# Kernel tuning notes

Hardware: AMD Instinct MI355X
Metric: run time of the kernel (lower is better)

The kernel has to match this reference:

```python
import jax, jax.numpy as jnp
import numpy as np

D = 1024        # embed_dim
H = 16          # num_heads
HD = D // H     # head_dim
R = 8           # LoRA rank
LORA_SCALE = 16.0 / R  # alpha / r
W_BITS = 8
A_BITS = 8


def fake_quant(x, bits):
    # symmetric per-tensor fake quantization with straight-through estimator
    qmax = 2.0 ** (bits - 1) - 1.0
    scale = jnp.maximum(jnp.max(jnp.abs(x)) / qmax, 1e-8)
    q = jnp.round(x / scale) * scale
    return x + jax.lax.stop_gradient(q - x)


def quant_lora_linear(x, W, b, A, B):
    # QuantizeLinear: fake-quant activations (a_bits) and weights (w_bits)
    base = jnp.matmul(fake_quant(x, A_BITS), fake_quant(W, W_BITS).T) + b
    # active LoRA adapter: x @ A^T @ B^T * scaling (dropout=0)
    lora = jnp.matmul(jnp.matmul(x, A.T), B.T) * LORA_SCALE
    return base + lora


def setup_inputs() -> dict:
    key = jax.random.key(0)
    ks = jax.random.split(key, 20)
    bsz, seq = 2, 2048
    inp = {
        "hidden_states": jax.random.normal(ks[0], (bsz, seq, D), jnp.float32),
        "attention_mask": jnp.ones((bsz, seq), jnp.float32),
    }
    i = 1
    for name in ("q", "k", "v", "out"):
        inp[f"{name}_W"] = jax.random.normal(ks[i], (D, D), jnp.float32) * 0.02; i += 1
        inp[f"{name}_b"] = jnp.zeros((D,), jnp.float32)
        inp[f"{name}_A"] = jax.random.normal(ks[i], (R, D), jnp.float32) * 0.01; i += 1
        inp[f"{name}_B"] = jax.random.normal(ks[i], (D, R), jnp.float32) * 0.01; i += 1
    return inp


def reference(hidden_states, attention_mask,
              q_W, q_b, q_A, q_B,
              k_W, k_b, k_A, k_B,
              v_W, v_b, v_A, v_B,
              out_W, out_b, out_A, out_B):
    bsz, seq, _ = hidden_states.shape

    q = quant_lora_linear(hidden_states, q_W, q_b, q_A, q_B)
    k = quant_lora_linear(hidden_states, k_W, k_b, k_A, k_B)
    v = quant_lora_linear(hidden_states, v_W, v_b, v_A, v_B)

    # (b, s, D) -> (b, H, s, HD)
    def shape_heads(x):
        return x.reshape(bsz, seq, H, HD).transpose(0, 2, 1, 3)

    q, k, v = shape_heads(q), shape_heads(k), shape_heads(v)

    scores = jnp.einsum("bhqd,bhkd->bhqk", q, k) / jnp.sqrt(jnp.float32(HD))
    # additive mask: (1 - mask) * -10000, broadcast over (b, 1, 1, s)
    scores = scores + (1.0 - attention_mask)[:, None, None, :] * -10000.0
    probs = jax.nn.softmax(scores, axis=-1)

    attn = jnp.einsum("bhqk,bhkd->bhqd", probs, v)
    attn = attn.transpose(0, 2, 1, 3).reshape(bsz, seq, D)
    return quant_lora_linear(attn, out_W, out_b, out_A, out_B)
```

## Files before the change

kernel.cpp:

```cpp
#include <hip/hip_runtime.h>
#include <stdint.h>

typedef __attribute__((ext_vector_type(8))) short short8;
typedef __attribute__((ext_vector_type(4))) float f32x4;
typedef __attribute__((ext_vector_type(4))) int int32x4;
typedef unsigned short ushort_t;
typedef signed char i8_t;

#define SEQ   2048
#define BSZ   2
#define DIM   1024
#define NHEAD 16
#define HDIM  64
#define MROWS (BSZ*SEQ)

__device__ __forceinline__ ushort_t f2bf(float f) {
  unsigned u = __float_as_uint(f);
  unsigned r = u + 0x7fffu + ((u >> 16) & 1u);
  return (ushort_t)(r >> 16);
}

__device__ __forceinline__ unsigned cvt_pk_bf16(float lo, float hi) {
  unsigned r;
  asm("v_cvt_pk_bf16_f32 %0, %1, %2" : "=v"(r) : "v"(lo), "v"(hi));
  return r;
}

__device__ __forceinline__ float fast_exp2(float x) {
#if __has_builtin(__builtin_amdgcn_exp2f)
  return __builtin_amdgcn_exp2f(x);
#else
  return exp2f(x);
#endif
}

__device__ __forceinline__ int pack4i8(float a, float b, float c, float d) {
  int ia = (int)rintf(a), ib = (int)rintf(b), ic = (int)rintf(c), id = (int)rintf(d);
  return (ia & 255) | ((ib & 255) << 8) | ((ic & 255) << 16) | (id << 24);
}

typedef __attribute__((address_space(1))) void gas_void;
typedef __attribute__((address_space(3))) void las_void;
__device__ __forceinline__ void gll16(const void* g, void* l, int lane) {
#if __has_builtin(__builtin_amdgcn_global_load_lds)
  __builtin_amdgcn_global_load_lds((gas_void*)g, (las_void*)l, 16, 0, 0);
#else
  ((int4*)l)[lane] = *(const int4*)g;
#endif
}

__device__ __forceinline__ void amax_reduce_store(float m, unsigned* slot) {
  __shared__ float wred[4];
  int wv = threadIdx.x >> 6, lane = threadIdx.x & 63;
#pragma unroll
  for (int off = 32; off > 0; off >>= 1) m = fmaxf(m, __shfl_down(m, off));
  if (lane == 0) wred[wv] = m;
  __syncthreads();
  if (threadIdx.x == 0) {
    float r = fmaxf(fmaxf(wred[0], wred[1]), fmaxf(wred[2], wred[3]));
    atomicMax(slot, __float_as_uint(r));
  }
}

__global__ __launch_bounds__(256) void amax5_kernel(
    const float* __restrict__ x, const float* w0, const float* w1,
    const float* w2, const float* w3, int n4x, int n4w,
    unsigned* __restrict__ slots) {
  int y = blockIdx.y;
  const float* p = (y == 0) ? x : (y == 1) ? w0 : (y == 2) ? w1 : (y == 3) ? w2 : w3;
  int n4 = (y == 0) ? n4x : n4w;
  const float4* x4 = (const float4*)p;
  float m = 0.f;
  for (int i = blockIdx.x * blockDim.x + threadIdx.x; i < n4; i += gridDim.x * blockDim.x) {
    float4 v = x4[i];
    m = fmaxf(m, fmaxf(fmaxf(fabsf(v.x), fabsf(v.y)), fmaxf(fabsf(v.z), fabsf(v.w))));
  }
  amax_reduce_store(m, slots + y);
}

__global__ __launch_bounds__(256) void quant4_kernel(const float* w0, const float* w1,
                                                     const float* w2, const float* w3,
                                                     i8_t* q0, i8_t* q1,
                                                     i8_t* q2, i8_t* q3,
                                                     int n4, const unsigned* __restrict__ slots) {
  int y = blockIdx.y;
  const float* x = (y == 0) ? w0 : (y == 1) ? w1 : (y == 2) ? w2 : w3;
  i8_t* qc = (y == 0) ? q0 : (y == 1) ? q1 : (y == 2) ? q2 : q3;
  float amax = __uint_as_float(slots[y + 1]);
  float s = fmaxf(amax / 127.0f, 1e-8f);
  float inv = 1.0f / s;
  const float4* x4 = (const float4*)x;
  int* q4 = (int*)qc;
  for (int i = blockIdx.x * blockDim.x + threadIdx.x; i < n4; i += gridDim.x * blockDim.x) {
    float4 v = x4[i];
    q4[i] = pack4i8(v.x * inv, v.y * inv, v.z * inv, v.w * inv);
  }
}

template <int NL>
__global__ __launch_bounds__(256) void lora_quant_kernel(
    const float* __restrict__ x, const unsigned* __restrict__ slot,
    i8_t* __restrict__ xc,
    const float* __restrict__ A0, const float* __restrict__ A1, const float* __restrict__ A2,
    float* __restrict__ t0, float* __restrict__ t1, float* __restrict__ t2) {
  const int row = blockIdx.x;
  const int tid = threadIdx.x;
  const int k0 = tid * 4;
  float amax = __uint_as_float(*slot);
  float s = fmaxf(amax / 127.0f, 1e-8f);
  float inv = 1.0f / s;

  float4 xv = *(const float4*)&x[(size_t)row * DIM + k0];
  *(int*)&xc[(size_t)row * DIM + k0] = pack4i8(xv.x * inv, xv.y * inv, xv.z * inv, xv.w * inv);

  float p[NL * 8];
#pragma unroll
  for (int r = 0; r < 8; r++) {
    float4 a = *(const float4*)&A0[r * DIM + k0];
    p[r] = xv.x * a.x + xv.y * a.y + xv.z * a.z + xv.w * a.w;
    if (NL > 1) {
      float4 a1 = *(const float4*)&A1[r * DIM + k0];
      p[8 + r] = xv.x * a1.x + xv.y * a1.y + xv.z * a1.z + xv.w * a1.w;
    }
    if (NL > 2) {
      float4 a2 = *(const float4*)&A2[r * DIM + k0];
      p[16 + r] = xv.x * a2.x + xv.y * a2.y + xv.z * a2.z + xv.w * a2.w;
    }
  }
#pragma unroll
  for (int j = 0; j < NL * 8; j++) {
    float v = p[j];
#pragma unroll
    for (int off = 32; off > 0; off >>= 1) v += __shfl_down(v, off);
    p[j] = v;
  }
  __shared__ float red[4][24];
  int wv = tid >> 6, lane = tid & 63;
  if (lane == 0) {
#pragma unroll
    for (int j = 0; j < NL * 8; j++) red[wv][j] = p[j];
  }
  __syncthreads();
  if (tid < NL * 8) {
    int j = tid;
    float sv = red[0][j] + red[1][j] + red[2][j] + red[3][j];
    float* tp = (j < 8) ? t0 : ((j < 16) ? t1 : t2);
    tp[(size_t)row * 8 + (j & 7)] = sv;
  }
}

template <bool BF16OUT, int BN>
__device__ __forceinline__ void proj_body(
    const i8_t* __restrict__ Ac, const i8_t* __restrict__ Wc,
    const unsigned* __restrict__ sxslot, const unsigned* __restrict__ swslot,
    const float* __restrict__ bias, const float* __restrict__ t,
    const float* __restrict__ Bl, void* __restrict__ Cout,
    int m0, int n0) {
  __shared__ alignas(16) i8_t Asb[128 * 128];
  __shared__ alignas(16) i8_t Bsb[BN * 128];
  __shared__ float Ts[128 * 8];
  __shared__ float Bls[BN * 8];
  __shared__ float biass[BN];

  const int tid = threadIdx.x;
  constexpr int NJ = BN / 32;
  constexpr int BITS = BN / 32;

  for (int i = tid; i < 128 * 8; i += 256) Ts[i] = t[(size_t)m0 * 8 + i];
  for (int i = tid; i < BN * 8; i += 256) Bls[i] = Bl[(size_t)n0 * 8 + i];
  if (tid < BN) biass[tid] = bias[n0 + tid];

  int32x4 acc[4][NJ];
#pragma unroll
  for (int i = 0; i < 4; i++)
#pragma unroll
    for (int j = 0; j < NJ; j++) {
      acc[i][j][0] = 0; acc[i][j][1] = 0; acc[i][j][2] = 0; acc[i][j][3] = 0;
    }

  const int wv = tid >> 6, lane = tid & 63;
  const int wr = wv >> 1, wc = wv & 1;
  const int l15 = lane & 15, hi = lane >> 4;
  const int lr8 = lane >> 3, lc8 = lane & 7;

  for (int kt = 0; kt < 8; kt++) {
    const int k0 = kt * 128;
#pragma unroll
    for (int j = 0; j < 4; j++) {
      int row = wv * 32 + j * 8 + lr8;
      int cs = lc8 ^ (row & 7);
      gll16(&Ac[(size_t)(m0 + row) * DIM + k0 + cs * 16], &Asb[(wv * 32 + j * 8) * 128], lane);
    }
#pragma unroll
    for (int j = 0; j < BITS; j++) {
      int row = wv * (BN / 4) + j * 8 + lr8;
      int cs = lc8 ^ (row & 7);
      gll16(&Wc[(size_t)(n0 + row) * DIM + k0 + cs * 16], &Bsb[(wv * (BN / 4) + j * 8) * 128], lane);
    }
    __syncthreads();
#pragma unroll
    for (int ks = 0; ks < 2; ks++) {
      int32x4 a[4], b[NJ];
#pragma unroll
      for (int i = 0; i < 4; i++) {
        int row = wr * 64 + i * 16 + l15;
        a[i] = *(const int32x4*)&Asb[row * 128 + (((ks * 4 + hi) ^ (row & 7))) * 16];
      }
#pragma unroll
      for (int j = 0; j < NJ; j++) {
        int col = wc * (BN / 2) + j * 16 + l15;
        b[j] = *(const int32x4*)&Bsb[col * 128 + (((ks * 4 + hi) ^ (col & 7))) * 16];
      }
      __builtin_amdgcn_s_setprio(1);
#pragma unroll
      for (int i = 0; i < 4; i++)
#pragma unroll
        for (int j = 0; j < NJ; j++)
          acc[i][j] = __builtin_amdgcn_mfma_i32_16x16x64_i8(a[i], b[j], acc[i][j], 0, 0, 0);
      __builtin_amdgcn_s_setprio(0);
    }
    __syncthreads();
  }

  float sx = fmaxf(__uint_as_float(*sxslot) / 127.0f, 1e-8f);
  float sw = fmaxf(__uint_as_float(*swslot) / 127.0f, 1e-8f);
  float ss = sx * sw;
#pragma unroll
  for (int i = 0; i < 4; i++) {
#pragma unroll
    for (int rr = 0; rr < 4; rr++) {
      int rl = wr * 64 + i * 16 + hi * 4 + rr;
      float tv[8];
#pragma unroll
      for (int q = 0; q < 8; q++) tv[q] = Ts[rl * 8 + q];
#pragma unroll
      for (int j = 0; j < NJ; j++) {
        int cl = wc * (BN / 2) + j * 16 + l15;
        float lr = 0.f;
#pragma unroll
        for (int q = 0; q < 8; q++) lr += tv[q] * Bls[cl * 8 + q];
        float val = (float)acc[i][j][rr] * ss + biass[cl] + 2.0f * lr;
        if (BF16OUT)
          ((ushort_t*)Cout)[(size_t)(m0 + rl) * DIM + n0 + cl] = f2bf(val);
        else
          ((float*)Cout)[(size_t)(m0 + rl) * DIM + n0 + cl] = val;
      }
    }
  }
}

struct ProjSet {
  const i8_t* W; const unsigned* sw; const float* bias;
  const float* t; const float* Bl; ushort_t* out;
};

__global__ __launch_bounds__(256) void proj_qkv_kernel(
    const i8_t* __restrict__ Ac, const unsigned* __restrict__ sxslot,
    ProjSet pq, ProjSet pk, ProjSet pv) {
  ProjSet P = (blockIdx.z == 0) ? pq : (blockIdx.z == 1) ? pk : pv;
  proj_body<true, 128>(Ac, P.W, sxslot, P.sw, P.bias, P.t, P.Bl, P.out,
                       blockIdx.y * 128, blockIdx.x * 128);
}

__global__ __launch_bounds__(256) void proj_out_kernel(
    const i8_t* __restrict__ Ac, const i8_t* __restrict__ Wc,
    const unsigned* __restrict__ sxslot, const unsigned* __restrict__ swslot,
    const float* __restrict__ bias, const float* __restrict__ t,
    const float* __restrict__ Bl, float* __restrict__ Cout) {
  proj_body<false, 64>(Ac, Wc, sxslot, swslot, bias, t, Bl, Cout,
                       blockIdx.y * 128, blockIdx.x * 64);
}

__global__ __launch_bounds__(256) void vtrans_kernel(const ushort_t* __restrict__ vb,
                                                     ushort_t* __restrict__ vT) {
  __shared__ alignas(16) ushort_t Lt[64 * 72];
  const int s0 = blockIdx.x * 64;
  const int bh = blockIdx.y;
  const int b = bh >> 4, h = bh & 15;
  const int tid = threadIdx.x;
#pragma unroll
  for (int it = 0; it < 2; it++) {
    int g = it * 256 + tid;
    int r = g >> 3, c = g & 7;
    *(int4*)&Lt[r * 72 + c * 8] =
        *(const int4*)&vb[(size_t)(b * SEQ + s0 + r) * DIM + h * 64 + c * 8];
  }
  __syncthreads();
#pragma unroll
  for (int it = 0; it < 2; it++) {
    int g = it * 256 + tid;
    int d = g >> 3, c = g & 7;
    union { int4 v; ushort_t u[8]; } out;
#pragma unroll
    for (int j = 0; j < 8; j++) out.u[j] = Lt[(c * 8 + j) * 72 + d];
    *(int4*)&vT[((size_t)bh * 64 + d) * SEQ + s0 + c * 8] = out.v;
  }
}

__global__ __launch_bounds__(256) void attn9_kernel(
    const ushort_t* __restrict__ qb, const ushort_t* __restrict__ kb,
    const ushort_t* __restrict__ vT, const float* __restrict__ mask,
    float* __restrict__ obuf, unsigned* __restrict__ amax_slot) {
  __shared__ alignas(16) ushort_t Ks[2][64 * 64];
  __shared__ alignas(16) ushort_t Vs[2][64 * 64];
  __shared__ alignas(16) ushort_t Ps[128 * 72];
  __shared__ alignas(16) float maskv[2][64];
  __shared__ float wmax[4];

  const float LOG2E = 1.44269504088896f;
  const float SCL2 = 0.125f * LOG2E;
  const float THR2 = 8.0f * LOG2E;

  const int lin = blockIdx.x;
  const int logical = (lin & 7) * 64 + (lin >> 3);
  const int bh = logical >> 4;
  const int qt = logical & 15;
  const int b = bh >> 4, h = bh & 15;
  const size_t tokbase = (size_t)b * SEQ;
  const int q0 = qt * 128;

  const int tid = threadIdx.x;
  const int wv = tid >> 6, lane = tid & 63, l15 = lane & 15, hi = lane >> 4;
  const int sr = tid >> 3, sc = tid & 7;
  const int sslot = (sc ^ (sr & 7)) * 8;
  const int sslot2 = (sc ^ ((sr + 32) & 7)) * 8;

  short8 qf[2][2];
#pragma unroll
  for (int rb = 0; rb < 2; rb++)
#pragma unroll
    for (int ks = 0; ks < 2; ks++) {
      int row = q0 + wv * 32 + rb * 16 + l15;
      qf[rb][ks] = *(const short8*)&qb[(tokbase + row) * DIM + h * 64 + ks * 32 + hi * 8];
    }

  float mo[2], ls[2];
  f32x4 o[2][4];
#pragma unroll
  for (int rb = 0; rb < 2; rb++) { mo[rb] = -1e30f; ls[rb] = 0.f; }
#pragma unroll
  for (int rb = 0; rb < 2; rb++)
#pragma unroll
    for (int d = 0; d < 4; d++) { o[rb][d][0] = 0.f; o[rb][d][1] = 0.f; o[rb][d][2] = 0.f; o[rb][d][3] = 0.f; }

  int4 kpre0, kpre1, vpre0, vpre1;
  float mpre;
  kpre0 = *(const int4*)&kb[(tokbase + sr) * DIM + h * 64 + sc * 8];
  vpre0 = *(const int4*)&vT[((size_t)bh * 64 + sr) * SEQ + sc * 8];
  kpre1 = *(const int4*)&kb[(tokbase + sr + 32) * DIM + h * 64 + sc * 8];
  vpre1 = *(const int4*)&vT[((size_t)bh * 64 + sr + 32) * SEQ + sc * 8];
  mpre = (tid < 64) ? (1.0f - mask[tokbase + tid]) * (-10000.0f * LOG2E) : 0.f;
  *(int4*)&Ks[0][sr * 64 + sslot] = kpre0;
  *(int4*)&Vs[0][sr * 64 + sslot] = vpre0;
  *(int4*)&Ks[0][(sr + 32) * 64 + sslot2] = kpre1;
  *(int4*)&Vs[0][(sr + 32) * 64 + sslot2] = vpre1;
  if (tid < 64) maskv[0][tid] = mpre;
  __syncthreads();

  for (int kt = 0; kt < 32; kt++) {
    const int cur = kt & 1, nxt = cur ^ 1;

    if (kt < 31) {
      const int k0n = (kt + 1) * 64;
      kpre0 = *(const int4*)&kb[(tokbase + k0n + sr) * DIM + h * 64 + sc * 8];
      vpre0 = *(const int4*)&vT[((size_t)bh * 64 + sr) * SEQ + k0n + sc * 8];
      kpre1 = *(const int4*)&kb[(tokbase + k0n + sr + 32) * DIM + h * 64 + sc * 8];
      vpre1 = *(const int4*)&vT[((size_t)bh * 64 + sr + 32) * SEQ + k0n + sc * 8];
      if (tid < 64) mpre = (1.0f - mask[tokbase + k0n + tid]) * (-10000.0f * LOG2E);
    }

    f32x4 s2[4][2];
#pragma unroll
    for (int kb4 = 0; kb4 < 4; kb4++)
#pragma unroll
      for (int rb = 0; rb < 2; rb++) { s2[kb4][rb][0] = 0.f; s2[kb4][rb][1] = 0.f; s2[kb4][rb][2] = 0.f; s2[kb4][rb][3] = 0.f; }
#pragma unroll
    for (int ks = 0; ks < 2; ks++) {
      short8 kf[4];
#pragma unroll
      for (int kb4 = 0; kb4 < 4; kb4++) {
        int row = kb4 * 16 + l15;
        kf[kb4] = *(const short8*)&Ks[cur][row * 64 + (((ks * 4 + hi) ^ (row & 7))) * 8];
      }
      __builtin_amdgcn_s_setprio(1);
#pragma unroll
      for (int kb4 = 0; kb4 < 4; kb4++)
#pragma unroll
        for (int rb = 0; rb < 2; rb++)
          s2[kb4][rb] = __builtin_amdgcn_mfma_f32_16x16x32_bf16(kf[kb4], qf[rb][ks], s2[kb4][rb], 0, 0, 0);
      __builtin_amdgcn_s_setprio(0);
    }

#pragma unroll
    for (int kb4 = 0; kb4 < 4; kb4++) {
      f32x4 mkv = *(const f32x4*)&maskv[cur][kb4 * 16 + hi * 4];
#pragma unroll
      for (int rb = 0; rb < 2; rb++)
#pragma unroll
        for (int r = 0; r < 4; r++)
          s2[kb4][rb][r] = s2[kb4][rb][r] * SCL2 + mkv[r];
    }

    float tm[2];
#pragma unroll
    for (int rb = 0; rb < 2; rb++) {
      float t0m = fmaxf(fmaxf(s2[0][rb][0], s2[0][rb][1]), fmaxf(s2[0][rb][2], s2[0][rb][3]));
      float t1m = fmaxf(fmaxf(s2[1][rb][0], s2[1][rb][1]), fmaxf(s2[1][rb][2], s2[1][rb][3]));
      float t2m = fmaxf(fmaxf(s2[2][rb][0], s2[2][rb][1]), fmaxf(s2[2][rb][2], s2[2][rb][3]));
      float t3m = fmaxf(fmaxf(s2[3][rb][0], s2[3][rb][1]), fmaxf(s2[3][rb][2], s2[3][rb][3]));
      float t = fmaxf(fmaxf(t0m, t1m), fmaxf(t2m, t3m));
      t = fmaxf(t, __shfl_xor(t, 16));
      t = fmaxf(t, __shfl_xor(t, 32));
      tm[rb] = t;
    }

    bool need = (tm[0] > mo[0] + THR2) || (tm[1] > mo[1] + THR2);
    if (__any(need)) {
      float al[2];
#pragma unroll
      for (int rb = 0; rb < 2; rb++) {
        float mn = fmaxf(mo[rb], tm[rb]);
        al[rb] = fast_exp2(mo[rb] - mn);
        mo[rb] = mn;
        ls[rb] *= al[rb];
      }
#pragma unroll
      for (int rb = 0; rb < 2; rb++)
#pragma unroll
        for (int r = 0; r < 4; r++) {
          float ab = __shfl(al[rb], hi * 4 + r);
#pragma unroll
          for (int db = 0; db < 4; db++) o[rb][db][r] *= ab;
        }
    }

#pragma unroll
    for (int rb = 0; rb < 2; rb++) {
      float rsv = 0.f;
#pragma unroll
      for (int kb4 = 0; kb4 < 4; kb4++)
#pragma unroll
        for (int r = 0; r < 4; r++) {
          float pv = fast_exp2(s2[kb4][rb][r] - mo[rb]);
          s2[kb4][rb][r] = pv;
          rsv += pv;
        }
      rsv += __shfl_xor(rsv, 16);
      rsv += __shfl_xor(rsv, 32);
      ls[rb] += rsv;
    }

#pragma unroll
    for (int rb = 0; rb < 2; rb++) {
      int rowb = (wv * 32 + rb * 16 + l15) * 72;
#pragma unroll
      for (int kb4 = 0; kb4 < 4; kb4++) {
        unsigned w0 = cvt_pk_bf16(s2[kb4][rb][0], s2[kb4][rb][1]);
        unsigned w1 = cvt_pk_bf16(s2[kb4][rb][2], s2[kb4][rb][3]);
        *(uint2*)&Ps[rowb + kb4 * 16 + hi * 4] = make_uint2(w0, w1);
      }
    }

#pragma unroll
    for (int ks = 0; ks < 2; ks++) {
      short8 pf[2];
#pragma unroll
      for (int rb = 0; rb < 2; rb++) {
        int row = wv * 32 + rb * 16 + l15;
        pf[rb] = *(const short8*)&Ps[row * 72 + ks * 32 + hi * 8];
      }
      short8 vf[4];
#pragma unroll
      for (int db = 0; db < 4; db++) {
        int row = db * 16 + l15;
        vf[db] = *(const short8*)&Vs[cur][row * 64 + (((ks * 4 + hi) ^ (row & 7))) * 8];
      }
      __builtin_amdgcn_s_setprio(1);
#pragma unroll
      for (int rb = 0; rb < 2; rb++)
#pragma unroll
        for (int db = 0; db < 4; db++)
          o[rb][db] = __builtin_amdgcn_mfma_f32_16x16x32_bf16(pf[rb], vf[db], o[rb][db], 0, 0, 0);
      __builtin_amdgcn_s_setprio(0);
    }

    if (kt < 31) {
      *(int4*)&Ks[nxt][sr * 64 + sslot] = kpre0;
      *(int4*)&Vs[nxt][sr * 64 + sslot] = vpre0;
      *(int4*)&Ks[nxt][(sr + 32) * 64 + sslot2] = kpre1;
      *(int4*)&Vs[nxt][(sr + 32) * 64 + sslot2] = vpre1;
      if (tid < 64) maskv[nxt][tid] = mpre;
    }
    __syncthreads();
  }

  float am = 0.f;
#pragma unroll
  for (int rb = 0; rb < 2; rb++)
#pragma unroll
    for (int r = 0; r < 4; r++) {
      float lsb = __shfl(ls[rb], hi * 4 + r);
      float inv = 1.0f / lsb;
      size_t row = tokbase + q0 + wv * 32 + rb * 16 + hi * 4 + r;
#pragma unroll
      for (int db = 0; db < 4; db++) {
        float val = o[rb][db][r] * inv;
        am = fmaxf(am, fabsf(val));
        obuf[row * DIM + h * 64 + db * 16 + l15] = val;
      }
    }
#pragma unroll
  for (int off = 32; off > 0; off >>= 1) am = fmaxf(am, __shfl_down(am, off));
  if (lane == 0) wmax[wv] = am;
  __syncthreads();
  if (tid == 0)
    atomicMax(amax_slot, __float_as_uint(fmaxf(fmaxf(wmax[0], wmax[1]), fmaxf(wmax[2], wmax[3]))));
}

extern "C" void kernel_launch(void* const* d_in, const int* in_sizes, int n_in,
                              void* d_out, int out_size, void* d_ws, size_t ws_size,
                              hipStream_t stream) {
  const float* x     = (const float*)d_in[0];
  const float* mask  = (const float*)d_in[1];
  const float* q_W   = (const float*)d_in[2];
  const float* q_b   = (const float*)d_in[3];
  const float* q_A   = (const float*)d_in[4];
  const float* q_B   = (const float*)d_in[5];
  const float* k_W   = (const float*)d_in[6];
  const float* k_b   = (const float*)d_in[7];
  const float* k_A   = (const float*)d_in[8];
  const float* k_B   = (const float*)d_in[9];
  const float* v_W   = (const float*)d_in[10];
  const float* v_b   = (const float*)d_in[11];
  const float* v_A   = (const float*)d_in[12];
  const float* v_B   = (const float*)d_in[13];
  const float* o_W   = (const float*)d_in[14];
  const float* o_b   = (const float*)d_in[15];
  const float* o_A   = (const float*)d_in[16];
  const float* o_B   = (const float*)d_in[17];
  float* out = (float*)d_out;

  char* ws = (char*)d_ws;
  const size_t MB = 1u << 20;
  unsigned* slots = (unsigned*)ws;
  float* t_q = (float*)(ws + 4096);
  float* t_k = t_q + MROWS * 8;
  float* t_v = t_k + MROWS * 8;
  float* t_o = t_v + MROWS * 8;
  i8_t* xc  = (i8_t*)(ws + 1 * MB);
  i8_t* qWc = (i8_t*)(ws + 9 * MB);
  i8_t* kWc = (i8_t*)(ws + 11 * MB);
  i8_t* vWc = (i8_t*)(ws + 13 * MB);
  i8_t* oWc = (i8_t*)(ws + 15 * MB);
  ushort_t* qbb = (ushort_t*)(ws + 17 * MB);
  ushort_t* kbb = (ushort_t*)(ws + 25 * MB);
  ushort_t* vbb = (ushort_t*)(ws + 33 * MB);
  ushort_t* vTb = (ushort_t*)(ws + 41 * MB);
  float*    abuf = (float*)(ws + 49 * MB);
  i8_t*     ac  = (i8_t*)(ws + 65 * MB);

  (void)hipMemsetAsync(ws, 0, 64, stream);

  const int NX4 = (MROWS * DIM) / 4;
  const int NW4 = (DIM * DIM) / 4;

  amax5_kernel<<<dim3(256, 5), 256, 0, stream>>>(x, q_W, k_W, v_W, o_W, NX4, NW4, slots);
  quant4_kernel<<<dim3(128, 4), 256, 0, stream>>>(q_W, k_W, v_W, o_W,
                                                  qWc, kWc, vWc, oWc, NW4, slots);

  lora_quant_kernel<3><<<MROWS, 256, 0, stream>>>(x, slots + 0, xc, q_A, k_A, v_A,
                                                  t_q, t_k, t_v);

  ProjSet pq = { qWc, slots + 1, q_b, t_q, q_B, qbb };
  ProjSet pk = { kWc, slots + 2, k_b, t_k, k_B, kbb };
  ProjSet pv = { vWc, slots + 3, v_b, t_v, v_B, vbb };
  proj_qkv_kernel<<<dim3(DIM / 128, MROWS / 128, 3), 256, 0, stream>>>(xc, slots + 0, pq, pk, pv);

  vtrans_kernel<<<dim3(SEQ / 64, BSZ * NHEAD), 256, 0, stream>>>(vbb, vTb);

  attn9_kernel<<<512, 256, 0, stream>>>(qbb, kbb, vTb, mask, abuf, slots + 5);

  lora_quant_kernel<1><<<MROWS, 256, 0, stream>>>(abuf, slots + 5, ac, o_A, nullptr, nullptr,
                                                  t_o, nullptr, nullptr);

  proj_out_kernel<<<dim3(DIM / 64, MROWS / 128), 256, 0, stream>>>(
      ac, oWc, slots + 5, slots + 4, o_b, t_o, o_B, out);
}
```

Baseline: 196.3 us.

## Fuse V transpose into QKV projection epilogue and merge weight quant with prep

The V projection epilogue now stages its bf16 tile transposed in shared memory and writes V directly in the head-major transposed layout, so the separate vtrans kernel and the intermediate V buffer round-trip go away. Weight quantization and the input quant plus LoRA-A kernel are merged into one launch with extra blocks, which saves a launch and lets the two overlap. Shared memory is now a unioned raw buffer so the transpose staging can reuse the operand tiles. In exchange, V blocks take a different epilogue path and the QKV kernel uses more shared memory.

```diff
diff --git a/kernel.cpp b/kernel.cpp
--- a/kernel.cpp
+++ b/kernel.cpp
@@ -78,89 +78,124 @@
   amax_reduce_store(m, slots + y);
 }
 
-__global__ __launch_bounds__(256) void quant4_kernel(const float* w0, const float* w1,
-                                                     const float* w2, const float* w3,
-                                                     i8_t* q0, i8_t* q1,
-                                                     i8_t* q2, i8_t* q3,
-                                                     int n4, const unsigned* __restrict__ slots) {
-  int y = blockIdx.y;
-  const float* x = (y == 0) ? w0 : (y == 1) ? w1 : (y == 2) ? w2 : w3;
-  i8_t* qc = (y == 0) ? q0 : (y == 1) ? q1 : (y == 2) ? q2 : q3;
-  float amax = __uint_as_float(slots[y + 1]);
-  float s = fmaxf(amax / 127.0f, 1e-8f);
-  float inv = 1.0f / s;
-  const float4* x4 = (const float4*)x;
-  int* q4 = (int*)qc;
-  for (int i = blockIdx.x * blockDim.x + threadIdx.x; i < n4; i += gridDim.x * blockDim.x) {
-    float4 v = x4[i];
-    q4[i] = pack4i8(v.x * inv, v.y * inv, v.z * inv, v.w * inv);
-  }
-}
-
-template <int NL>
-__global__ __launch_bounds__(256) void lora_quant_kernel(
-    const float* __restrict__ x, const unsigned* __restrict__ slot,
+__global__ __launch_bounds__(256) void prep_kernel(
+    const float* __restrict__ x, const unsigned* __restrict__ slots,
     i8_t* __restrict__ xc,
     const float* __restrict__ A0, const float* __restrict__ A1, const float* __restrict__ A2,
-    float* __restrict__ t0, float* __restrict__ t1, float* __restrict__ t2) {
+    float* __restrict__ t0, float* __restrict__ t1, float* __restrict__ t2,
+    const float* w0, const float* w1, const float* w2, const float* w3,
+    i8_t* q0, i8_t* q1, i8_t* q2, i8_t* q3, int n4w) {
+  const int tid = threadIdx.x;
+  if ((int)blockIdx.x >= MROWS) {
+    int wb = blockIdx.x - MROWS;
+    int y = wb >> 7, bx = wb & 127;
+    const float* wsrc = (y == 0) ? w0 : (y == 1) ? w1 : (y == 2) ? w2 : w3;
+    i8_t* qc = (y == 0) ? q0 : (y == 1) ? q1 : (y == 2) ? q2 : q3;
+    float amax = __uint_as_float(slots[y + 1]);
+    float inv = 1.0f / fmaxf(amax / 127.0f, 1e-8f);
+    const float4* x4 = (const float4*)wsrc;
+    int* q4 = (int*)qc;
+    for (int i = bx * 256 + tid; i < n4w; i += 128 * 256) {
+      float4 v = x4[i];
+      q4[i] = pack4i8(v.x * inv, v.y * inv, v.z * inv, v.w * inv);
+    }
+    return;
+  }
+  const int row = blockIdx.x;
+  const int k0 = tid * 4;
+  float amax = __uint_as_float(slots[0]);
+  float inv = 1.0f / fmaxf(amax / 127.0f, 1e-8f);
+
+  float4 xv = *(const float4*)&x[(size_t)row * DIM + k0];
+  *(int*)&xc[(size_t)row * DIM + k0] = pack4i8(xv.x * inv, xv.y * inv, xv.z * inv, xv.w * inv);
+
+  float p[24];
+#pragma unroll
+  for (int r = 0; r < 8; r++) {
+    float4 a = *(const float4*)&A0[r * DIM + k0];
+    p[r] = xv.x * a.x + xv.y * a.y + xv.z * a.z + xv.w * a.w;
+    float4 a1 = *(const float4*)&A1[r * DIM + k0];
+    p[8 + r] = xv.x * a1.x + xv.y * a1.y + xv.z * a1.z + xv.w * a1.w;
+    float4 a2 = *(const float4*)&A2[r * DIM + k0];
+    p[16 + r] = xv.x * a2.x + xv.y * a2.y + xv.z * a2.z + xv.w * a2.w;
+  }
+#pragma unroll
+  for (int j = 0; j < 24; j++) {
+    float v = p[j];
+#pragma unroll
+    for (int off = 32; off > 0; off >>= 1) v += __shfl_down(v, off);
+    p[j] = v;
+  }
+  __shared__ float red[4][24];
+  int wv = tid >> 6, lane = tid & 63;
+  if (lane == 0) {
+#pragma unroll
+    for (int j = 0; j < 24; j++) red[wv][j] = p[j];
+  }
+  __syncthreads();
+  if (tid < 24) {
+    int j = tid;
+    float sv = red[0][j] + red[1][j] + red[2][j] + red[3][j];
+    float* tp = (j < 8) ? t0 : ((j < 16) ? t1 : t2);
+    tp[(size_t)row * 8 + (j & 7)] = sv;
+  }
+}
+
+__global__ __launch_bounds__(256) void lora_quant1_kernel(
+    const float* __restrict__ x, const unsigned* __restrict__ slot,
+    i8_t* __restrict__ xc, const float* __restrict__ A0, float* __restrict__ t0) {
   const int row = blockIdx.x;
   const int tid = threadIdx.x;
   const int k0 = tid * 4;
   float amax = __uint_as_float(*slot);
-  float s = fmaxf(amax / 127.0f, 1e-8f);
-  float inv = 1.0f / s;
+  float inv = 1.0f / fmaxf(amax / 127.0f, 1e-8f);
 
   float4 xv = *(const float4*)&x[(size_t)row * DIM + k0];
   *(int*)&xc[(size_t)row * DIM + k0] = pack4i8(xv.x * inv, xv.y * inv, xv.z * inv, xv.w * inv);
 
-  float p[NL * 8];
+  float p[8];
 #pragma unroll
   for (int r = 0; r < 8; r++) {
     float4 a = *(const float4*)&A0[r * DIM + k0];
     p[r] = xv.x * a.x + xv.y * a.y + xv.z * a.z + xv.w * a.w;
-    if (NL > 1) {
-      float4 a1 = *(const float4*)&A1[r * DIM + k0];
-      p[8 + r] = xv.x * a1.x + xv.y * a1.y + xv.z * a1.z + xv.w * a1.w;
-    }
-    if (NL > 2) {
-      float4 a2 = *(const float4*)&A2[r * DIM + k0];
-      p[16 + r] = xv.x * a2.x + xv.y * a2.y + xv.z * a2.z + xv.w * a2.w;
-    }
-  }
-#pragma unroll
-  for (int j = 0; j < NL * 8; j++) {
+  }
+#pragma unroll
+  for (int j = 0; j < 8; j++) {
     float v = p[j];
 #pragma unroll
     for (int off = 32; off > 0; off >>= 1) v += __shfl_down(v, off);
     p[j] = v;
   }
-  __shared__ float red[4][24];
+  __shared__ float red[4][8];
   int wv = tid >> 6, lane = tid & 63;
   if (lane == 0) {
 #pragma unroll
-    for (int j = 0; j < NL * 8; j++) red[wv][j] = p[j];
+    for (int j = 0; j < 8; j++) red[wv][j] = p[j];
   }
   __syncthreads();
-  if (tid < NL * 8) {
+  if (tid < 8) {
     int j = tid;
-    float sv = red[0][j] + red[1][j] + red[2][j] + red[3][j];
-    float* tp = (j < 8) ? t0 : ((j < 16) ? t1 : t2);
-    tp[(size_t)row * 8 + (j & 7)] = sv;
-  }
-}
-
-template <bool BF16OUT, int BN>
+    t0[(size_t)row * 8 + j] = red[0][j] + red[1][j] + red[2][j] + red[3][j];
+  }
+}
+
+template <bool BF16OUT, int BN, bool CANTRANS>
 __device__ __forceinline__ void proj_body(
     const i8_t* __restrict__ Ac, const i8_t* __restrict__ Wc,
     const unsigned* __restrict__ sxslot, const unsigned* __restrict__ swslot,
     const float* __restrict__ bias, const float* __restrict__ t,
     const float* __restrict__ Bl, void* __restrict__ Cout,
-    int m0, int n0) {
-  __shared__ alignas(16) i8_t Asb[128 * 128];
-  __shared__ alignas(16) i8_t Bsb[BN * 128];
-  __shared__ float Ts[128 * 8];
-  __shared__ float Bls[BN * 8];
-  __shared__ float biass[BN];
+    ushort_t* __restrict__ vTout, int m0, int n0) {
+  constexpr int CODEB = 128 * 128 + BN * 128;
+  constexpr int T2B = CANTRANS ? 128 * 136 * 2 : 0;
+  constexpr int BASE = (T2B > CODEB) ? T2B : CODEB;
+  __shared__ alignas(16) char smem[BASE + 128 * 32 + BN * 32 + BN * 4];
+  i8_t* Asb = (i8_t*)smem;
+  i8_t* Bsb = (i8_t*)(smem + 128 * 128);
+  ushort_t* T2 = (ushort_t*)smem;
+  float* Ts = (float*)(smem + BASE);
+  float* Bls = Ts + 128 * 8;
+  float* biass = Bls + BN * 8;
 
   const int tid = threadIdx.x;
   constexpr int NJ = BN / 32;
@@ -225,6 +260,48 @@
   float sx = fmaxf(__uint_as_float(*sxslot) / 127.0f, 1e-8f);
   float sw = fmaxf(__uint_as_float(*swslot) / 127.0f, 1e-8f);
   float ss = sx * sw;
+
+  if (CANTRANS && vTout != nullptr) {
+#pragma unroll
+    for (int i = 0; i < 4; i++) {
+      int rl0 = wr * 64 + i * 16 + hi * 4;
+      float tv[4][8];
+#pragma unroll
+      for (int rr = 0; rr < 4; rr++)
+#pragma unroll
+        for (int q = 0; q < 8; q++) tv[rr][q] = Ts[(rl0 + rr) * 8 + q];
+#pragma unroll
+      for (int j = 0; j < NJ; j++) {
+        int cl = wc * (BN / 2) + j * 16 + l15;
+        float val[4];
+#pragma unroll
+        for (int rr = 0; rr < 4; rr++) {
+          float lr = 0.f;
+#pragma unroll
+          for (int q = 0; q < 8; q++) lr += tv[rr][q] * Bls[cl * 8 + q];
+          val[rr] = (float)acc[i][j][rr] * ss + biass[cl] + 2.0f * lr;
+        }
+        unsigned w0 = cvt_pk_bf16(val[0], val[1]);
+        unsigned w1 = cvt_pk_bf16(val[2], val[3]);
+        *(uint2*)&T2[cl * 136 + rl0] = make_uint2(w0, w1);
+      }
+    }
+    __syncthreads();
+    const int bb = m0 >> 11;
+    const int sbase = m0 & 2047;
+#pragma unroll
+    for (int it = 0; it < 8; it++) {
+      int g = it * 256 + tid;
+      int d = g >> 4, c = g & 15;
+      int gdim = n0 + d;
+      int hh = gdim >> 6, dd = gdim & 63;
+      int bh = bb * 16 + hh;
+      int4 v = *(const int4*)&T2[d * 136 + c * 8];
+      *(int4*)&vTout[((size_t)(bh * 64 + dd)) * SEQ + sbase + c * 8] = v;
+    }
+    return;
+  }
+
 #pragma unroll
   for (int i = 0; i < 4; i++) {
 #pragma unroll
@@ -256,10 +333,11 @@
 
 __global__ __launch_bounds__(256) void proj_qkv_kernel(
     const i8_t* __restrict__ Ac, const unsigned* __restrict__ sxslot,
-    ProjSet pq, ProjSet pk, ProjSet pv) {
+    ProjSet pq, ProjSet pk, ProjSet pv, ushort_t* __restrict__ vT) {
   ProjSet P = (blockIdx.z == 0) ? pq : (blockIdx.z == 1) ? pk : pv;
-  proj_body<true, 128>(Ac, P.W, sxslot, P.sw, P.bias, P.t, P.Bl, P.out,
-                       blockIdx.y * 128, blockIdx.x * 128);
+  ushort_t* vt = (blockIdx.z == 2) ? vT : nullptr;
+  proj_body<true, 128, true>(Ac, P.W, sxslot, P.sw, P.bias, P.t, P.Bl, P.out,
+                             vt, blockIdx.y * 128, blockIdx.x * 128);
 }
 
 __global__ __launch_bounds__(256) void proj_out_kernel(
@@ -267,34 +345,8 @@
     const unsigned* __restrict__ sxslot, const unsigned* __restrict__ swslot,
     const float* __restrict__ bias, const float* __restrict__ t,
     const float* __restrict__ Bl, float* __restrict__ Cout) {
-  proj_body<false, 64>(Ac, Wc, sxslot, swslot, bias, t, Bl, Cout,
-                       blockIdx.y * 128, blockIdx.x * 64);
-}
-
-__global__ __launch_bounds__(256) void vtrans_kernel(const ushort_t* __restrict__ vb,
-                                                     ushort_t* __restrict__ vT) {
-  __shared__ alignas(16) ushort_t Lt[64 * 72];
-  const int s0 = blockIdx.x * 64;
-  const int bh = blockIdx.y;
-  const int b = bh >> 4, h = bh & 15;
-  const int tid = threadIdx.x;
-#pragma unroll
-  for (int it = 0; it < 2; it++) {
-    int g = it * 256 + tid;
-    int r = g >> 3, c = g & 7;
-    *(int4*)&Lt[r * 72 + c * 8] =
-        *(const int4*)&vb[(size_t)(b * SEQ + s0 + r) * DIM + h * 64 + c * 8];
-  }
-  __syncthreads();
-#pragma unroll
-  for (int it = 0; it < 2; it++) {
-    int g = it * 256 + tid;
-    int d = g >> 3, c = g & 7;
-    union { int4 v; ushort_t u[8]; } out;
-#pragma unroll
-    for (int j = 0; j < 8; j++) out.u[j] = Lt[(c * 8 + j) * 72 + d];
-    *(int4*)&vT[((size_t)bh * 64 + d) * SEQ + s0 + c * 8] = out.v;
-  }
+  proj_body<false, 64, false>(Ac, Wc, sxslot, swslot, bias, t, Bl, Cout,
+                              nullptr, blockIdx.y * 128, blockIdx.x * 64);
 }
 
 __global__ __launch_bounds__(256) void attn9_kernel(
@@ -554,7 +606,6 @@
   i8_t* oWc = (i8_t*)(ws + 15 * MB);
   ushort_t* qbb = (ushort_t*)(ws + 17 * MB);
   ushort_t* kbb = (ushort_t*)(ws + 25 * MB);
-  ushort_t* vbb = (ushort_t*)(ws + 33 * MB);
   ushort_t* vTb = (ushort_t*)(ws + 41 * MB);
   float*    abuf = (float*)(ws + 49 * MB);
   i8_t*     ac  = (i8_t*)(ws + 65 * MB);
@@ -565,23 +616,21 @@
   const int NW4 = (DIM * DIM) / 4;
 
   amax5_kernel<<<dim3(256, 5), 256, 0, stream>>>(x, q_W, k_W, v_W, o_W, NX4, NW4, slots);
-  quant4_kernel<<<dim3(128, 4), 256, 0, stream>>>(q_W, k_W, v_W, o_W,
-                                                  qWc, kWc, vWc, oWc, NW4, slots);
-
-  lora_quant_kernel<3><<<MROWS, 256, 0, stream>>>(x, slots + 0, xc, q_A, k_A, v_A,
-                                                  t_q, t_k, t_v);
+
+  prep_kernel<<<MROWS + 512, 256, 0, stream>>>(x, slots, xc, q_A, k_A, v_A,
+                                               t_q, t_k, t_v,
+                                               q_W, k_W, v_W, o_W,
+                                               qWc, kWc, vWc, oWc, NW4);
 
   ProjSet pq = { qWc, slots + 1, q_b, t_q, q_B, qbb };
   ProjSet pk = { kWc, slots + 2, k_b, t_k, k_B, kbb };
-  ProjSet pv = { vWc, slots + 3, v_b, t_v, v_B, vbb };
-  proj_qkv_kernel<<<dim3(DIM / 128, MROWS / 128, 3), 256, 0, stream>>>(xc, slots + 0, pq, pk, pv);
-
-  vtrans_kernel<<<dim3(SEQ / 64, BSZ * NHEAD), 256, 0, stream>>>(vbb, vTb);
+  ProjSet pv = { vWc, slots + 3, v_b, t_v, v_B, nullptr };
+  proj_qkv_kernel<<<dim3(DIM / 128, MROWS / 128, 3), 256, 0, stream>>>(
+      xc, slots + 0, pq, pk, pv, vTb);
 
   attn9_kernel<<<512, 256, 0, stream>>>(qbb, kbb, vTb, mask, abuf, slots + 5);
 
-  lora_quant_kernel<1><<<MROWS, 256, 0, stream>>>(abuf, slots + 5, ac, o_A, nullptr, nullptr,
-                                                  t_o, nullptr, nullptr);
+  lora_quant1_kernel<<<MROWS, 256, 0, stream>>>(abuf, slots + 5, ac, o_A, t_o);
 
   proj_out_kernel<<<dim3(DIM / 64, MROWS / 128), 256, 0, stream>>>(
       ac, oWc, slots + 5, slots + 4, o_b, t_o, o_B, out);
```

After: 184.2 us. -6.1%, faster.
